# Kernel optimization log

Hardware: AMD Instinct MI355X
Metric: run time of the kernel (lower is better)

Reference implementation:

```python
import jax, jax.numpy as jnp
import numpy as np

PLP_ORDER = 16
N_CHANNEL = 40
FFT_LENGTH = 512
SAMPLE_RATE = 16000
LIFTER = 22
COMP_FACTOR = 0.33
FLOOR = 1e-5
F_MIN = 0.0
F_MAX = SAMPLE_RATE / 2


def _hz_to_mel(hz):
    return 1127.0 * np.log1p(np.asarray(hz, dtype=np.float64) / 700.0)


def _mel_to_hz(mel):
    return 700.0 * np.expm1(np.asarray(mel, dtype=np.float64) / 1127.0)


def _build_constants():
    # SPTK-style mel filter bank (triangular in mel domain).
    mel_min = _hz_to_mel(F_MIN)
    mel_max = _hz_to_mel(F_MAX)
    lower_bin = max(1, int(F_MIN / SAMPLE_RATE * FFT_LENGTH + 1.5))
    upper_bin = min(FFT_LENGTH // 2, int(F_MAX / SAMPLE_RATE * FFT_LENGTH + 0.5))
    seed = np.arange(1, N_CHANNEL + 2)
    cf_mel = (mel_max - mel_min) / (N_CHANNEL + 1) * seed + mel_min  # (C+1,)
    bins = np.arange(lower_bin, upper_bin)
    mel = _hz_to_mel(SAMPLE_RATE * bins / FFT_LENGTH)
    ch = np.searchsorted(cf_mel, mel, side='left')  # first center freq >= mel
    diff = cf_mel - np.concatenate([[mel_min], cf_mel[:-1]])
    w = (cf_mel[ch] - mel) / diff[ch]
    H = np.zeros((len(bins), N_CHANNEL))
    rows = np.arange(len(bins))
    low = ch - 1
    m_lo = low >= 0
    H[rows[m_lo], low[m_lo]] += w[m_lo]
    m_hi = ch <= N_CHANNEL - 1
    H[rows[m_hi], ch[m_hi]] += 1.0 - w[m_hi]
    # Equal-loudness curve over the first C center frequencies (in Hz).
    cf_hz = _mel_to_hz(cf_mel)
    f2 = cf_hz[:N_CHANNEL] ** 2
    eql = (f2 / (f2 + 160000.0)) ** 2 * (f2 + 1440000.0) / (f2 + 9610000.0)
    # Liftering vector, v[0] = 2.
    m = np.arange(PLP_ORDER + 1)
    lift = 1.0 + LIFTER / 2.0 * np.sin(np.pi / LIFTER * m)
    lift[0] = 2.0
    return lower_bin, upper_bin, H.astype(np.float32), eql.astype(np.float32), lift.astype(np.float32)


LOWER_BIN, UPPER_BIN, H_NP, EQL_NP, LIFT_NP = _build_constants()


def _levinson_durbin(r):
    # r: (..., M+1) autocorrelation -> (gain K, LPC coefficients a_1..a_M)
    M = PLP_ORDER
    E = r[..., 0]
    a = jnp.zeros(r.shape[:-1] + (M,), r.dtype)
    for i in range(1, M + 1):
        acc = r[..., i]
        if i > 1:
            acc = acc + jnp.einsum('...j,...j->...', a[..., : i - 1], r[..., 1:i][..., ::-1])
        k = -acc / E
        if i > 1:
            a = a.at[..., : i - 1].set(a[..., : i - 1] + k[..., None] * a[..., : i - 1][..., ::-1])
        a = a.at[..., i - 1].set(k)
        E = E * (1.0 - k * k)
    return jnp.sqrt(E), a


def _lpc_to_cepstrum(K, a):
    # c0 = log K; c_m = -a_m - sum_{k=1}^{m-1} (k/m) c_k a_{m-k}
    M = PLP_ORDER
    c = [jnp.log(K)]
    for m in range(1, M + 1):
        acc = a[..., m - 1]
        for k in range(1, m):
            acc = acc + (k / m) * c[k] * a[..., m - k - 1]
        c.append(-acc)
    return jnp.stack(c, axis=-1)  # (..., M+1)


def _plp(x):
    H = jnp.asarray(H_NP)
    eql = jnp.asarray(EQL_NP)
    lift = jnp.asarray(LIFT_NP)
    # Mel filter bank on power spectrum (use_power=True)
    fb = jnp.matmul(x[..., LOWER_BIN:UPPER_BIN], H)          # (..., C)
    logfb = jnp.log(jnp.maximum(fb, FLOOR))
    # Equal-loudness scaling + cubic-root amplitude compression
    y = (jnp.exp(logfb) * eql) ** COMP_FACTOR                # (..., C)
    # replicate1: duplicate first and last channels
    y = jnp.concatenate([y[..., :1], y, y[..., -1:]], axis=-1)  # (..., C+2)
    n = y.shape[-1]
    # hfft with norm='forward' -> inverse-FFT-like autocorrelation
    r = jnp.fft.hfft(y) / (2 * (n - 1))
    r = r[..., : PLP_ORDER + 1]
    K, a = _levinson_durbin(r)
    c = _lpc_to_cepstrum(K, a)
    c = c * lift
    return c[..., 1:]  # out_format 'y': PLP without C0, (..., M)


def setup_inputs() -> dict:
    key = jax.random.key(0)
    x = jax.random.uniform(key, (32, 4096, FFT_LENGTH // 2 + 1), dtype=jnp.float32)
    return {"x": x}


def reference(x):
    return _plp(x)
```

## Files before the change

### kernel.cpp

```cpp
#include <hip/hip_runtime.h>
#include <hip/hip_fp16.h>

#define NCH   40
#define MORD  16
#define NR    17
#define NBINS 257
#define FPB   128
#define FSTR  258

namespace cfg {

constexpr double PI  = 3.14159265358979323846264338327950288;
constexpr double LN2 = 0.693147180559945309417232121458176568;

constexpr double cexp(double x) {
    double t = 1.0, s = 1.0;
    for (int i = 1; i < 40; ++i) { t *= x / i; s += t; }
    return s;
}

constexpr double clog(double z) {
    double lg = 0.0;
    while (z > 1.4142135623730951) { z *= 0.5; lg += LN2; }
    while (z < 0.7071067811865476) { z *= 2.0; lg -= LN2; }
    double u = (z - 1.0) / (z + 1.0), u2 = u * u, t = u, s = u;
    for (int k = 1; k < 24; ++k) { t *= u2; s += t / (2.0 * k + 1.0); }
    return lg + 2.0 * s;
}

constexpr double ccos(double x) {
    double tp = 2.0 * PI;
    double q = x / tp;
    long long k = (long long)(q + (q >= 0.0 ? 0.5 : -0.5));
    double r = x - (double)k * tp;
    double r2 = r * r, t = 1.0, s = 1.0;
    for (int i = 1; i < 20; ++i) { t *= -r2 / ((2.0 * i - 1.0) * (2.0 * i)); s += t; }
    return s;
}

constexpr double csin(double x) { return ccos(x - PI / 2.0); }

struct Tab {
    int   start[43];
    int   chan[257];
    float w[257];
    float eql[NCH];
    float lift[NR];
    float ctf[NR][21];
    constexpr Tab() : start(), chan(), w(), eql(), lift(), ctf() {
        const double lmax  = clog(87.0 / 7.0);
        const double U1127 = lmax / 41.0;
        for (int c = 0; c <= 41; ++c) {
            double thr = 22.4 * (cexp((double)c * U1127) - 1.0);
            int s = (int)thr + 1;
            if (s < 1) s = 1;
            if (s > 256) s = 256;
            start[c] = s;
        }
        start[42] = start[41];
        for (int c = 0; c <= 40; ++c) {
            for (int b = start[c]; b < start[c + 1]; ++b) {
                double mel = 1127.0 * clog(1.0 + (double)b * 31.25 / 700.0);
                double t   = mel / (1127.0 * U1127);
                w[b] = (float)(t - (double)c);
                chan[b] = c;
            }
        }
        for (int c = 0; c < NCH; ++c) {
            double cf = 700.0 * (cexp((double)(c + 1) * U1127) - 1.0);
            double f2 = cf * cf;
            double e  = f2 / (f2 + 160000.0);
            e = e * e * (f2 + 1440000.0) / (f2 + 9610000.0);
            eql[c] = (float)e;
        }
        for (int m = 0; m < NR; ++m)
            lift[m] = (float)(1.0 + 11.0 * csin(PI * (double)m / 22.0));
        lift[0] = 2.0f;
        for (int l = 0; l < NR; ++l)
            for (int j = 0; j <= 20; ++j) {
                double s = (j == 0) ? 1.0 : 2.0;
                ctf[l][j] = (float)(s * ccos(PI * (double)(j * l) / 41.0) / 82.0);
            }
    }
};

constexpr Tab T{};

}

__global__ __launch_bounds__(FPB) void plp_kernel(const float* __restrict__ x,
                                                  float* __restrict__ out,
                                                  int nframes)
{
    using cfg::T;
    __shared__ __half slab[FPB * FSTR];
    const int tid = threadIdx.x;
    const long long F0 = (long long)blockIdx.x * FPB;

    {
        const int s  = tid >> 6;
        const int ll = tid & 63;
        __half2* l2 = reinterpret_cast<__half2*>(slab);
        #pragma unroll 8
        for (int r = 0; r < 64; ++r) {
            const int fl = 2 * r + s;
            long long fg = F0 + fl;
            if (fg > (long long)nframes - 1) fg = (long long)nframes - 1;
            const float* g = x + fg * NBINS + 1 + 4 * ll;
            float x0 = g[0], x1 = g[1], x2 = g[2], x3 = g[3];
            const int d = fl * 129 + 2 * ll;
            l2[d]     = __float22half2_rn(make_float2(x0, x1));
            l2[d + 1] = __float22half2_rn(make_float2(x2, x3));
        }
    }
    __syncthreads();

    const long long frame = F0 + tid;
    if (frame >= nframes) return;
    const __half2* fr2 = reinterpret_cast<const __half2*>(slab) + tid * 129;

    float fb[NCH];
    #pragma unroll
    for (int c = 0; c < NCH; ++c) fb[c] = 0.f;

    #pragma unroll
    for (int p = 0; p < 128; ++p) {
        float2 xp = __half22float2(fr2[p]);
        {
            constexpr int b = 1;
            (void)b;
        }
        {
            const int   bb = 2 * p + 1;
            const int   c  = T.chan[bb];
            const float wa = T.w[bb];
            if (c < 40) fb[c]     = fmaf(wa, xp.x, fb[c]);
            if (c >= 1) fb[c - 1] = fmaf(1.0f - wa, xp.x, fb[c - 1]);
        }
        if (2 * p + 2 <= 255) {
            const int   bb = 2 * p + 2;
            const int   c  = T.chan[bb];
            const float wa = T.w[bb];
            if (c < 40) fb[c]     = fmaf(wa, xp.y, fb[c]);
            if (c >= 1) fb[c - 1] = fmaf(1.0f - wa, xp.y, fb[c - 1]);
        }
    }

    float yv[NCH];
    #pragma unroll
    for (int c = 0; c < NCH; ++c) {
        float v = fmaxf(fb[c], 1e-5f) * T.eql[c];
        yv[c] = __expf(0.33f * __logf(v));
    }

    float ye[21], yo[21];
    ye[0] = yv[0] + yv[39];  yo[0] = yv[0] - yv[39];
    #pragma unroll
    for (int j = 1; j <= 20; ++j) {
        float aa = yv[j - 1], bb = yv[40 - j];
        ye[j] = aa + bb;  yo[j] = aa - bb;
    }

    float r[NR];
    #pragma unroll
    for (int l = 0; l < NR; ++l) {
        const float* yy = (l & 1) ? yo : ye;
        float acc = 0.f;
        #pragma unroll
        for (int j = 0; j <= 20; ++j) acc = fmaf(T.ctf[l][j], yy[j], acc);
        r[l] = acc;
    }

    float a[MORD];
    #pragma unroll
    for (int i = 0; i < MORD; ++i) a[i] = 0.f;
    float E = r[0];
    #pragma unroll
    for (int i = 1; i <= MORD; ++i) {
        float acc = r[i];
        #pragma unroll
        for (int j = 0; j < i - 1; ++j) acc = fmaf(a[j], r[i - 1 - j], acc);
        float k = -acc * __builtin_amdgcn_rcpf(E);
        const int half = (i - 1) / 2;
        #pragma unroll
        for (int j = 0; j < half; ++j) {
            float t1 = a[j], t2 = a[i - 2 - j];
            a[j]         = fmaf(k, t2, t1);
            a[i - 2 - j] = fmaf(k, t1, t2);
        }
        if ((i - 1) & 1) a[half] = fmaf(k, a[half], a[half]);
        a[i - 1] = k;
        E = E * (1.f - k * k);
    }

    float cc[NR], ccs[NR];
    #pragma unroll
    for (int m = 1; m <= MORD; ++m) {
        float acc = 0.f;
        #pragma unroll
        for (int k2 = 1; k2 < m; ++k2)
            acc = fmaf(ccs[k2], a[m - k2 - 1], acc);
        float cm = -(a[m - 1] + acc * (1.0f / (float)m));
        cc[m]  = cm;
        ccs[m] = (float)m * cm;
    }

    float o[16];
    #pragma unroll
    for (int m = 1; m <= MORD; ++m) o[m - 1] = cc[m] * T.lift[m];

    float4* op = reinterpret_cast<float4*>(out + (size_t)frame * 16);
    op[0] = make_float4(o[0],  o[1],  o[2],  o[3]);
    op[1] = make_float4(o[4],  o[5],  o[6],  o[7]);
    op[2] = make_float4(o[8],  o[9],  o[10], o[11]);
    op[3] = make_float4(o[12], o[13], o[14], o[15]);
}

extern "C" void kernel_launch(void* const* d_in, const int* in_sizes, int n_in,
                              void* d_out, int out_size, void* d_ws, size_t ws_size,
                              hipStream_t stream) {
    const float* x   = (const float*)d_in[0];
    float*      outp = (float*)d_out;
    int nframes = in_sizes[0] / NBINS;
    int nblocks = (nframes + FPB - 1) / FPB;
    plp_kernel<<<nblocks, FPB, 0, stream>>>(x, outp, nframes);
}
```

Baseline: 194.9 us.

## Stream input via double-buffered global_load_lds chunks and coalesce output through LDS

```diff
diff --git a/kernel.cpp b/kernel.cpp
--- a/kernel.cpp
+++ b/kernel.cpp
@@ -1,12 +1,13 @@
 #include <hip/hip_runtime.h>
-#include <hip/hip_fp16.h>
-
-#define NCH   40
-#define MORD  16
-#define NR    17
-#define NBINS 257
-#define FPB   128
-#define FSTR  258
+
+#define NCH    40
+#define MORD   16
+#define NR     17
+#define NBINS  257
+#define FPB    128
+#define NCHUNK 8
+#define PAIRW  65
+#define OSTR   21
 
 namespace cfg {
 
@@ -88,62 +89,64 @@
 
 }
 
-__global__ __launch_bounds__(FPB) void plp_kernel(const float* __restrict__ x,
-                                                  float* __restrict__ out,
-                                                  int nframes)
+__device__ __forceinline__ void gload_lds4(const float* g, float* l) {
+    __builtin_amdgcn_global_load_lds(
+        (const __attribute__((address_space(1))) unsigned int*)g,
+        (__attribute__((address_space(3))) unsigned int*)l, 4, 0, 0);
+}
+
+__global__ __launch_bounds__(FPB, 2) void plp_kernel(const float* __restrict__ x,
+                                                     float* __restrict__ out,
+                                                     int nframes)
 {
     using cfg::T;
-    __shared__ __half slab[FPB * FSTR];
+    __shared__ float slab[2][64][PAIRW];
+
     const int tid = threadIdx.x;
     const long long F0 = (long long)blockIdx.x * FPB;
 
-    {
-        const int s  = tid >> 6;
-        const int ll = tid & 63;
-        __half2* l2 = reinterpret_cast<__half2*>(slab);
-        #pragma unroll 8
-        for (int r = 0; r < 64; ++r) {
-            const int fl = 2 * r + s;
-            long long fg = F0 + fl;
+    const int w = tid >> 6;
+    const int l = tid & 63;
+    const int s = l >> 5;
+    const int j = l & 31;
+
+    auto stage = [&](int c, int b) {
+        const float* gp0 = x + (c << 5) + j;
+        #pragma unroll
+        for (int r = 0; r < 32; ++r) {
+            const int g = (w << 5) + r;
+            long long fg = F0 + 2 * g + s;
             if (fg > (long long)nframes - 1) fg = (long long)nframes - 1;
-            const float* g = x + fg * NBINS + 1 + 4 * ll;
-            float x0 = g[0], x1 = g[1], x2 = g[2], x3 = g[3];
-            const int d = fl * 129 + 2 * ll;
-            l2[d]     = __float22half2_rn(make_float2(x0, x1));
-            l2[d + 1] = __float22half2_rn(make_float2(x2, x3));
-        }
-    }
+            gload_lds4(gp0 + fg * NBINS, &slab[b][g][0]);
+        }
+    };
+
+    stage(0, 0);
+
+    const int u   = tid >> 1;
+    const int v32 = (tid & 1) << 5;
+
+    float fb[NCH];
+    #pragma unroll
+    for (int c = 0; c < NCH; ++c) fb[c] = 0.f;
+
     __syncthreads();
 
-    const long long frame = F0 + tid;
-    if (frame >= nframes) return;
-    const __half2* fr2 = reinterpret_cast<const __half2*>(slab) + tid * 129;
-
-    float fb[NCH];
-    #pragma unroll
-    for (int c = 0; c < NCH; ++c) fb[c] = 0.f;
-
-    #pragma unroll
-    for (int p = 0; p < 128; ++p) {
-        float2 xp = __half22float2(fr2[p]);
-        {
-            constexpr int b = 1;
-            (void)b;
-        }
-        {
-            const int   bb = 2 * p + 1;
-            const int   c  = T.chan[bb];
+    #pragma unroll
+    for (int c8 = 0; c8 < NCHUNK; ++c8) {
+        if (c8 + 1 < NCHUNK) stage(c8 + 1, (c8 + 1) & 1);
+        const float* fr = &slab[c8 & 1][u][v32];
+        #pragma unroll
+        for (int p = 0; p < 32; ++p) {
+            const int bb = (c8 << 5) + p;
+            if (bb == 0) continue;
+            const float xv = fr[p];
+            const int   ch = T.chan[bb];
             const float wa = T.w[bb];
-            if (c < 40) fb[c]     = fmaf(wa, xp.x, fb[c]);
-            if (c >= 1) fb[c - 1] = fmaf(1.0f - wa, xp.x, fb[c - 1]);
-        }
-        if (2 * p + 2 <= 255) {
-            const int   bb = 2 * p + 2;
-            const int   c  = T.chan[bb];
-            const float wa = T.w[bb];
-            if (c < 40) fb[c]     = fmaf(wa, xp.y, fb[c]);
-            if (c >= 1) fb[c - 1] = fmaf(1.0f - wa, xp.y, fb[c - 1]);
-        }
+            if (ch < NCH) fb[ch]     = fmaf(wa, xv, fb[ch]);
+            if (ch >= 1)  fb[ch - 1] = fmaf(1.0f - wa, xv, fb[ch - 1]);
+        }
+        if (c8 + 1 < NCHUNK) __syncthreads();
     }
 
     float yv[NCH];
@@ -156,19 +159,19 @@
     float ye[21], yo[21];
     ye[0] = yv[0] + yv[39];  yo[0] = yv[0] - yv[39];
     #pragma unroll
-    for (int j = 1; j <= 20; ++j) {
-        float aa = yv[j - 1], bb = yv[40 - j];
-        ye[j] = aa + bb;  yo[j] = aa - bb;
+    for (int jj = 1; jj <= 20; ++jj) {
+        float aa = yv[jj - 1], bb = yv[40 - jj];
+        ye[jj] = aa + bb;  yo[jj] = aa - bb;
     }
 
     float r[NR];
     #pragma unroll
-    for (int l = 0; l < NR; ++l) {
-        const float* yy = (l & 1) ? yo : ye;
+    for (int lg = 0; lg < NR; ++lg) {
+        const float* yy = (lg & 1) ? yo : ye;
         float acc = 0.f;
         #pragma unroll
-        for (int j = 0; j <= 20; ++j) acc = fmaf(T.ctf[l][j], yy[j], acc);
-        r[l] = acc;
+        for (int jj = 0; jj <= 20; ++jj) acc = fmaf(T.ctf[lg][jj], yy[jj], acc);
+        r[lg] = acc;
     }
 
     float a[MORD];
@@ -179,14 +182,14 @@
     for (int i = 1; i <= MORD; ++i) {
         float acc = r[i];
         #pragma unroll
-        for (int j = 0; j < i - 1; ++j) acc = fmaf(a[j], r[i - 1 - j], acc);
+        for (int jj = 0; jj < i - 1; ++jj) acc = fmaf(a[jj], r[i - 1 - jj], acc);
         float k = -acc * __builtin_amdgcn_rcpf(E);
         const int half = (i - 1) / 2;
         #pragma unroll
-        for (int j = 0; j < half; ++j) {
-            float t1 = a[j], t2 = a[i - 2 - j];
-            a[j]         = fmaf(k, t2, t1);
-            a[i - 2 - j] = fmaf(k, t1, t2);
+        for (int jj = 0; jj < half; ++jj) {
+            float t1 = a[jj], t2 = a[i - 2 - jj];
+            a[jj]         = fmaf(k, t2, t1);
+            a[i - 2 - jj] = fmaf(k, t1, t2);
         }
         if ((i - 1) & 1) a[half] = fmaf(k, a[half], a[half]);
         a[i - 1] = k;
@@ -205,15 +208,25 @@
         ccs[m] = (float)m * cm;
     }
 
-    float o[16];
-    #pragma unroll
-    for (int m = 1; m <= MORD; ++m) o[m - 1] = cc[m] * T.lift[m];
-
-    float4* op = reinterpret_cast<float4*>(out + (size_t)frame * 16);
-    op[0] = make_float4(o[0],  o[1],  o[2],  o[3]);
-    op[1] = make_float4(o[4],  o[5],  o[6],  o[7]);
-    op[2] = make_float4(o[8],  o[9],  o[10], o[11]);
-    op[3] = make_float4(o[12], o[13], o[14], o[15]);
+    float* ob = &slab[0][0][0];
+    #pragma unroll
+    for (int m = 1; m <= MORD; ++m)
+        ob[tid * OSTR + (m - 1)] = cc[m] * T.lift[m];
+    __syncthreads();
+
+    float4* out4 = (float4*)out;
+    const long long gbase4 = F0 << 2;
+    const long long lim4   = ((long long)nframes) << 2;
+    #pragma unroll
+    for (int q = 0; q < 4; ++q) {
+        const int g4 = (q << 7) + tid;
+        const long long gi = gbase4 + g4;
+        if (gi < lim4) {
+            const int fr2 = g4 >> 2, e = g4 & 3;
+            const float* rb = &ob[fr2 * OSTR + (e << 2)];
+            out4[gi] = make_float4(rb[0], rb[1], rb[2], rb[3]);
+        }
+    }
 }
 
 extern "C" void kernel_launch(void* const* d_in, const int* in_sizes, int n_in,
```

Result: slower. 199.7 us (+2.5%).
